# Kernel tuning notes

Measured on AMD Instinct MI355X. Metric: run time of the kernel, lower is better.

Reference implementation:

```python
import jax, jax.numpy as jnp
import numpy as np

BS, NQ, NK = 4096, 21, 7   # batch, num_neg queries, 7 keys (weekdays)
E = 512                     # key_size == query_size
H = 512                     # hidden_size
NEG_INF = -1e9


def setup_inputs() -> dict:
    key = jax.random.key(0)
    ks = jax.random.split(key, 6)
    sq = 1.0 / np.sqrt(E)
    sh = 1.0 / np.sqrt(H)
    return {
        "queries": jax.random.normal(ks[0], (BS, NQ, E), jnp.float32),
        "keys": jax.random.normal(ks[1], (BS, NK, E), jnp.float32),
        "wq_w": jax.random.normal(ks[2], (H, E), jnp.float32) * sq,
        "wq_b": jnp.zeros((H,), jnp.float32),
        "wk_w": jax.random.normal(ks[3], (H, E), jnp.float32) * sq,
        "wk_b": jnp.zeros((H,), jnp.float32),
        "wv_w": jax.random.normal(ks[4], (1, H), jnp.float32) * sh,
        "wv_b": jnp.zeros((1,), jnp.float32),
        "cum_subs_masks": jax.random.randint(ks[5], (BS, 1, NK, 1), 0, 2).astype(jnp.int32),
        "num_neg": NQ,
    }


def reference(queries, keys, wq_w, wq_b, wk_w, wk_b, wv_w, wv_b, cum_subs_masks, num_neg):
    # dropout p=0.0 -> identity (as in eval / p=0)
    q = jnp.einsum('bqe,he->bqh', queries, wq_w) + wq_b          # (bs,21,H)
    k = jnp.einsum('bke,he->bkh', keys, wk_w) + wk_b             # (bs,7,H)
    # additive score: broadcast q over keys, k over queries
    t = jnp.tanh(q[:, :, None, :] + k[:, None, :, :])            # (bs,21,7,H)
    scores = jnp.einsum('bqkh,oh->bqko', t, wv_w) + wv_b         # (bs,21,7,1)
    scores = scores + cum_subs_masks.astype(scores.dtype) * NEG_INF
    attn_weights = jax.nn.softmax(scores, axis=-2)               # softmax over 7 keys
    # weighted sum of the RAW keys (the module multiplies by expanded `keys`)
    attn_out = jnp.einsum('bqk,bke->bqe', attn_weights[..., 0], keys)  # (bs,21,E)
    return (attn_out, attn_weights)
```

## Files before the change

kernel.cpp:

```cpp
#include <hip/hip_runtime.h>
#include <hip/hip_bf16.h>

#define BS_   4096
#define NQ_   21
#define NK_   7
#define E_    512
#define MQ_   (BS_*NQ_)
#define MK_   (BS_*NK_)
#define MT1_  (MQ_/128)
#define MT2_  (MK_/128)
#define SCALE_ 2.88539008177792681f

typedef __attribute__((ext_vector_type(8))) short bf16x8;
typedef __attribute__((ext_vector_type(4))) float f32x4;
typedef __attribute__((ext_vector_type(8))) unsigned short u16x8;

__device__ __forceinline__ unsigned int cvt_pk_bf16(float lo, float hi){
  unsigned int r;
  asm("v_cvt_pk_bf16_f32 %0, %1, %2" : "=v"(r) : "v"(lo), "v"(hi));
  return r;
}
__device__ __forceinline__ float bf2f(unsigned short h){
  return __builtin_bit_cast(float, (unsigned int)h << 16);
}
__device__ __forceinline__ void gload_lds16(const void* g, void* l){
  __builtin_amdgcn_global_load_lds(
      (const __attribute__((address_space(1))) unsigned int*)g,
      (__attribute__((address_space(3))) unsigned int*)l, 16, 0, 0);
}

__global__ __launch_bounds__(256) void cast_weights(
    const float* __restrict__ wq, const float* __restrict__ wk,
    unsigned int* __restrict__ oq, unsigned int* __restrict__ ok)
{
  int i = blockIdx.x * 256 + threadIdx.x;
  float4 a = ((const float4*)wq)[i];
  float4 b = ((const float4*)wk)[i];
  uint2 ua = { cvt_pk_bf16(a.x, a.y), cvt_pk_bf16(a.z, a.w) };
  uint2 ub = { cvt_pk_bf16(b.x, b.y), cvt_pk_bf16(b.z, b.w) };
  ((uint2*)oq)[i] = ua;
  ((uint2*)ok)[i] = ub;
}

__global__ __launch_bounds__(256)
void gemm_proj(const float* __restrict__ Aq, const float* __restrict__ Ak,
               const unsigned short* __restrict__ Bq, const unsigned short* __restrict__ Bk,
               const float* __restrict__ bq, const float* __restrict__ bk,
               unsigned short* __restrict__ Cq, unsigned short* __restrict__ Ck)
{
  __shared__ char Asm[3][128 * 64];
  __shared__ char Bsm[3][128 * 64];

  const int tid  = threadIdx.x;
  const int lane = tid & 63;
  const int w    = tid >> 6;
  const int wr   = w >> 1, wc = w & 1;

  const int orig = (int)blockIdx.x;
  const int j    = orig >> 3;
  int       mt   = (j >> 2) * 8 + (orig & 7);
  const int nt   = j & 3;

  const float* A; const unsigned short* Bw; const float* bias; unsigned short* C;
  if (mt < MT1_){ A = Aq; Bw = Bq; bias = bq; C = Cq; }
  else          { A = Ak; Bw = Bk; bias = bk; C = Ck; mt -= MT1_; }

  const long m0 = (long)mt << 7;
  const int  n0 = nt << 7;
  const char* Abyte = (const char*)(A + m0 * E_);
  const char* Bbyte = (const char*)Bw;

  long asrc[4]; int adst[4];
#pragma unroll
  for (int i = 0; i < 4; ++i){
    const int c   = tid + i * 256;
    const int row = c >> 3;
    const int sl  = c & 7;
    asrc[i] = (long)row * (E_ * 4) + sl * 16;
    adst[i] = row * 64 + (((sl & 6) * 8) ^ (((row >> 1) & 3) << 4)) + (sl & 1) * 8;
  }
  long bsrc[2]; int bdst[2];
#pragma unroll
  for (int i = 0; i < 2; ++i){
    const int c   = tid + i * 256;
    const int row = c >> 2;
    const int sl  = c & 3;
    bsrc[i] = (long)(n0 + row) * (E_ * 2) + ((sl * 16) ^ (((row >> 1) & 3) << 4));
    bdst[i] = c * 16;
  }

  int aoff[4], boff[4];
#pragma unroll
  for (int m = 0; m < 4; ++m){
    const int r = wr * 64 + m * 16 + (lane & 15);
    aoff[m] = r * 64 + ((16 * (lane >> 4)) ^ (((r >> 1) & 3) << 4));
  }
#pragma unroll
  for (int n = 0; n < 4; ++n){
    const int r = wc * 64 + n * 16 + (lane & 15);
    boff[n] = r * 64 + ((16 * (lane >> 4)) ^ (((r >> 1) & 3) << 4));
  }

  f32x4 acc[4][4];
  const f32x4 z4 = {0.f, 0.f, 0.f, 0.f};
#pragma unroll
  for (int m = 0; m < 4; ++m)
#pragma unroll
    for (int n = 0; n < 4; ++n) acc[m][n] = z4;

#define STAGE_LOADS(av, T) do { \
  _Pragma("unroll") for (int i_ = 0; i_ < 4; ++i_) \
    av[i_] = *(const float4*)(Abyte + asrc[i_] + (long)(T) * 128); \
} while(0)

#define STAGE_B(BUF, T) do { \
  _Pragma("unroll") for (int i_ = 0; i_ < 2; ++i_) \
    gload_lds16(Bbyte + bsrc[i_] + (long)(T) * 64, Bsm[BUF] + bdst[i_]); \
} while(0)

#define WRITE_A(BUF, av) do { \
  _Pragma("unroll") for (int i_ = 0; i_ < 4; ++i_){ \
    uint2 u_ = { cvt_pk_bf16(av[i_].x, av[i_].y), cvt_pk_bf16(av[i_].z, av[i_].w) }; \
    *(uint2*)(Asm[BUF] + adst[i_]) = u_; \
  } \
} while(0)

#define COMPUTE(BUF) do { \
  bf16x8 af_[4], bfr_[4]; \
  _Pragma("unroll") for (int m_ = 0; m_ < 4; ++m_) af_[m_]  = *(const bf16x8*)(Asm[BUF] + aoff[m_]); \
  _Pragma("unroll") for (int n_ = 0; n_ < 4; ++n_) bfr_[n_] = *(const bf16x8*)(Bsm[BUF] + boff[n_]); \
  _Pragma("unroll") for (int m_ = 0; m_ < 4; ++m_) \
    _Pragma("unroll") for (int n_ = 0; n_ < 4; ++n_) \
      acc[m_][n_] = __builtin_amdgcn_mfma_f32_16x16x32_bf16(af_[m_], bfr_[n_], acc[m_][n_], 0, 0, 0); \
} while(0)

#define BARRIER() do { \
  asm volatile("" ::: "memory"); \
  __builtin_amdgcn_s_barrier(); \
  asm volatile("" ::: "memory"); \
} while(0)

  float4 avA[4], avB[4];

  STAGE_LOADS(avA, 0);  STAGE_B(0, 0);
  STAGE_LOADS(avB, 1);  STAGE_B(1, 1);
  asm volatile("s_waitcnt vmcnt(6)" ::: "memory");
  WRITE_A(0, avA);

#pragma unroll
  for (int t = 0; t < 14; ++t){
    const int cur = t % 3, nx1 = (t + 1) % 3, nx2 = (t + 2) % 3;
    asm volatile("s_waitcnt vmcnt(2)" ::: "memory");
    if ((t & 1) == 0) WRITE_A(nx1, avB); else WRITE_A(nx1, avA);
    asm volatile("s_waitcnt lgkmcnt(0)" ::: "memory");
    BARRIER();
    if ((t & 1) == 0) STAGE_LOADS(avA, t + 2); else STAGE_LOADS(avB, t + 2);
    STAGE_B(nx2, t + 2);
    COMPUTE(cur);
  }
  {
    asm volatile("s_waitcnt vmcnt(2)" ::: "memory");
    WRITE_A(0 , avB);
    asm volatile("s_waitcnt lgkmcnt(0)" ::: "memory");
    BARRIER();
    COMPUTE(2 );
  }
  {
    asm volatile("s_waitcnt vmcnt(0)" ::: "memory");
    BARRIER();
    COMPUTE(0 );
  }

#undef STAGE_LOADS
#undef STAGE_B
#undef WRITE_A
#undef COMPUTE
#undef BARRIER

  const int ccol0 = n0 + wc * 64 + (lane & 15);
  float bvs[4];
#pragma unroll
  for (int n = 0; n < 4; ++n) bvs[n] = bias[ccol0 + n * 16] * SCALE_;
#pragma unroll
  for (int m = 0; m < 4; ++m){
    const long rbase = m0 + wr * 64 + m * 16 + (lane >> 4) * 4;
#pragma unroll
    for (int n = 0; n < 4; ++n){
      const long col = ccol0 + n * 16;
      float v0 = fmaf(acc[m][n][0], SCALE_, bvs[n]);
      float v1 = fmaf(acc[m][n][1], SCALE_, bvs[n]);
      float v2 = fmaf(acc[m][n][2], SCALE_, bvs[n]);
      float v3 = fmaf(acc[m][n][3], SCALE_, bvs[n]);
      unsigned int u01 = cvt_pk_bf16(v0, v1);
      unsigned int u23 = cvt_pk_bf16(v2, v3);
      C[(rbase + 0) * E_ + col] = (unsigned short)(u01 & 0xffffu);
      C[(rbase + 1) * E_ + col] = (unsigned short)(u01 >> 16);
      C[(rbase + 2) * E_ + col] = (unsigned short)(u23 & 0xffffu);
      C[(rbase + 3) * E_ + col] = (unsigned short)(u23 >> 16);
    }
  }
}

__global__ __launch_bounds__(256, 2)
void attn_fused(const unsigned short* __restrict__ qp,
                const unsigned short* __restrict__ kp,
                const float* __restrict__ keys,
                const float* __restrict__ wv, const float* __restrict__ wvb,
                const int* __restrict__ mask,
                float* __restrict__ out0, float* __restrict__ out1)
{
  const int lane = threadIdx.x & 63;
  const int b    = blockIdx.x * 4 + (threadIdx.x >> 6);

  float wvr[8];
  *(float4*)&wvr[0] = ((const float4*)wv)[lane * 2];
  *(float4*)&wvr[4] = ((const float4*)wv)[lane * 2 + 1];

  float kf[NK_][8];
#pragma unroll
  for (int k = 0; k < NK_; ++k){
    u16x8 u = *(const u16x8*)(kp + ((long)b * NK_ + k) * E_ + lane * 8);
#pragma unroll
    for (int j = 0; j < 8; ++j) kf[k][j] = bf2f((unsigned short)u[j]);
  }
  float kr[NK_][8];
#pragma unroll
  for (int k = 0; k < NK_; ++k){
    const float4* p = (const float4*)(keys + ((long)b * NK_ + k) * E_ + lane * 8);
    *(float4*)&kr[k][0] = p[0];
    *(float4*)&kr[k][4] = p[1];
  }

  float wsum = ((wvr[0] + wvr[1]) + (wvr[2] + wvr[3])) + ((wvr[4] + wvr[5]) + (wvr[6] + wvr[7]));
#pragma unroll
  for (int off = 32; off; off >>= 1) wsum += __shfl_xor(wsum, off, 64);

  const float vb = wvb[0];
  float base[NK_];
#pragma unroll
  for (int k = 0; k < NK_; ++k)
    base[k] = (wsum + vb) + (float)mask[b * NK_ + k] * (-1e9f);

  const unsigned short* qrow = qp + (long)b * NQ_ * E_ + lane * 8;
  u16x8 qv = *(const u16x8*)qrow;

  float4* o0 = (float4*)(out0 + (long)b * NQ_ * E_) + lane * 2;
  float*  o1 = out1 + (long)b * (NQ_ * NK_);

  for (int qi = 0; qi < NQ_; ++qi){
    u16x8 qn = qv;
    if (qi < NQ_ - 1) qn = *(const u16x8*)(qrow + (qi + 1) * E_);

    float qf[8];
#pragma unroll
    for (int j = 0; j < 8; ++j) qf[j] = bf2f((unsigned short)qv[j]);
    qv = qn;

    float acc[NK_];
#pragma unroll
    for (int k = 0; k < NK_; ++k){
      float a = 0.f;
#pragma unroll
      for (int j = 0; j < 8; ++j){
        float x = qf[j] + kf[k][j];
        float e = __builtin_amdgcn_exp2f(x);
        float r = __builtin_amdgcn_rcpf(e + 1.0f);
        a = fmaf(wvr[j], r, a);
      }
      acc[k] = a;
    }
#pragma unroll
    for (int k = 0; k < NK_; ++k){
      float a = acc[k];
#pragma unroll
      for (int off = 32; off; off >>= 1) a += __shfl_xor(a, off, 64);
      acc[k] = a;
    }
    float sc[NK_], mx = -3.4e38f;
#pragma unroll
    for (int k = 0; k < NK_; ++k){ sc[k] = fmaf(-2.f, acc[k], base[k]); mx = fmaxf(mx, sc[k]); }
    float sum = 0.f;
#pragma unroll
    for (int k = 0; k < NK_; ++k){ sc[k] = __expf(sc[k] - mx); sum += sc[k]; }
    const float inv = __builtin_amdgcn_rcpf(sum);
    float wgt[NK_];
#pragma unroll
    for (int k = 0; k < NK_; ++k) wgt[k] = sc[k] * inv;

    float wsel = wgt[0];
#pragma unroll
    for (int k = 1; k < NK_; ++k) wsel = (lane == k) ? wgt[k] : wsel;
    if (lane < NK_) o1[qi * NK_ + lane] = wsel;

    float4 lo = {0.f,0.f,0.f,0.f}, hi = {0.f,0.f,0.f,0.f};
#pragma unroll
    for (int k = 0; k < NK_; ++k){
      lo.x = fmaf(wgt[k], kr[k][0], lo.x);
      lo.y = fmaf(wgt[k], kr[k][1], lo.y);
      lo.z = fmaf(wgt[k], kr[k][2], lo.z);
      lo.w = fmaf(wgt[k], kr[k][3], lo.w);
      hi.x = fmaf(wgt[k], kr[k][4], hi.x);
      hi.y = fmaf(wgt[k], kr[k][5], hi.y);
      hi.z = fmaf(wgt[k], kr[k][6], hi.z);
      hi.w = fmaf(wgt[k], kr[k][7], hi.w);
    }
    o0[qi * 128 + 0] = lo;
    o0[qi * 128 + 1] = hi;
  }
}

extern "C" void kernel_launch(void* const* d_in, const int* in_sizes, int n_in,
                              void* d_out, int out_size, void* d_ws, size_t ws_size,
                              hipStream_t stream)
{
  const float* queries = (const float*)d_in[0];
  const float* keys    = (const float*)d_in[1];
  const float* wq_w    = (const float*)d_in[2];
  const float* wq_b    = (const float*)d_in[3];
  const float* wk_w    = (const float*)d_in[4];
  const float* wk_b    = (const float*)d_in[5];
  const float* wv_w    = (const float*)d_in[6];
  const float* wv_b    = (const float*)d_in[7];
  const int*   mask    = (const int*)d_in[8];
  (void)in_sizes; (void)n_in; (void)out_size; (void)ws_size;

  float* out0 = (float*)d_out;
  float* out1 = out0 + (long)MQ_ * E_;

  char* ws = (char*)d_ws;
  unsigned short* wqb = (unsigned short*)ws;
  unsigned short* wkb = (unsigned short*)(ws + 512 * 512 * 2);
  unsigned short* qb  = (unsigned short*)(ws + (1 << 20));
  unsigned short* kb  = qb + (size_t)MQ_ * E_;

  cast_weights<<<dim3(256), dim3(256), 0, stream>>>(wq_w, wk_w, (unsigned int*)wqb, (unsigned int*)wkb);
  gemm_proj<<<dim3((MT1_ + MT2_) * 4), dim3(256), 0, stream>>>(
      queries, keys, wqb, wkb, wq_b, wk_b, qb, kb);
  attn_fused<<<dim3(BS_ / 4), dim3(256), 0, stream>>>(qb, kb, keys, wv_w, wv_b, mask, out0, out1);
}
```

Before: 249.0 us.

## Restructure projection GEMM to 64-row tiles with B fragments loaded directly into registers

The projection GEMM moves from 128x128 tiles with triple-buffered LDS for both operands to 64x256 tiles. Each wave owns a 64-column slice and reads its weight fragments straight from global memory into registers, one k-step ahead. Only the A tile still goes through LDS, now double-buffered and smaller, which cuts LDS traffic and footprint and may allow higher occupancy. The cost is that weight fragments are re-read from global or L2 by every block instead of being shared through LDS, and the grid shape changes.

```diff
diff --git a/kernel.cpp b/kernel.cpp
--- a/kernel.cpp
+++ b/kernel.cpp
@@ -7,8 +7,9 @@
 #define E_    512
 #define MQ_   (BS_*NQ_)
 #define MK_   (BS_*NK_)
-#define MT1_  (MQ_/128)
-#define MT2_  (MK_/128)
+#define MTQ_  (MQ_/64)
+#define MTK_  (MK_/64)
+#define MTT_  (MTQ_+MTK_)
 #define SCALE_ 2.88539008177792681f
 
 typedef __attribute__((ext_vector_type(8))) short bf16x8;
@@ -22,11 +23,6 @@
 }
 __device__ __forceinline__ float bf2f(unsigned short h){
   return __builtin_bit_cast(float, (unsigned int)h << 16);
-}
-__device__ __forceinline__ void gload_lds16(const void* g, void* l){
-  __builtin_amdgcn_global_load_lds(
-      (const __attribute__((address_space(1))) unsigned int*)g,
-      (__attribute__((address_space(3))) unsigned int*)l, 16, 0, 0);
 }
 
 __global__ __launch_bounds__(256) void cast_weights(
@@ -48,58 +44,41 @@
                const float* __restrict__ bq, const float* __restrict__ bk,
                unsigned short* __restrict__ Cq, unsigned short* __restrict__ Ck)
 {
-  __shared__ char Asm[3][128 * 64];
-  __shared__ char Bsm[3][128 * 64];
+  __shared__ char Asm[2][64 * 64];
 
   const int tid  = threadIdx.x;
   const int lane = tid & 63;
   const int w    = tid >> 6;
-  const int wr   = w >> 1, wc = w & 1;
-
-  const int orig = (int)blockIdx.x;
-  const int j    = orig >> 3;
-  int       mt   = (j >> 2) * 8 + (orig & 7);
-  const int nt   = j & 3;
+
+  const int bid = (int)blockIdx.x;
+  const int j   = bid >> 3;
+  int       mt  = (j >> 1) * 8 + (bid & 7);
+  const int ntb = j & 1;
 
   const float* A; const unsigned short* Bw; const float* bias; unsigned short* C;
-  if (mt < MT1_){ A = Aq; Bw = Bq; bias = bq; C = Cq; }
-  else          { A = Ak; Bw = Bk; bias = bk; C = Ck; mt -= MT1_; }
-
-  const long m0 = (long)mt << 7;
-  const int  n0 = nt << 7;
+  if (mt < MTQ_){ A = Aq; Bw = Bq; bias = bq; C = Cq; }
+  else          { A = Ak; Bw = Bk; bias = bk; C = Ck; mt -= MTQ_; }
+
+  const long m0  = (long)mt << 6;
+  const int  n0w = ntb * 256 + w * 64;
   const char* Abyte = (const char*)(A + m0 * E_);
-  const char* Bbyte = (const char*)Bw;
-
-  long asrc[4]; int adst[4];
-#pragma unroll
-  for (int i = 0; i < 4; ++i){
+
+  long asrc[2]; int adst[2];
+#pragma unroll
+  for (int i = 0; i < 2; ++i){
     const int c   = tid + i * 256;
     const int row = c >> 3;
     const int sl  = c & 7;
     asrc[i] = (long)row * (E_ * 4) + sl * 16;
     adst[i] = row * 64 + (((sl & 6) * 8) ^ (((row >> 1) & 3) << 4)) + (sl & 1) * 8;
   }
-  long bsrc[2]; int bdst[2];
-#pragma unroll
-  for (int i = 0; i < 2; ++i){
-    const int c   = tid + i * 256;
-    const int row = c >> 2;
-    const int sl  = c & 3;
-    bsrc[i] = (long)(n0 + row) * (E_ * 2) + ((sl * 16) ^ (((row >> 1) & 3) << 4));
-    bdst[i] = c * 16;
-  }
-
-  int aoff[4], boff[4];
+  int aoff[4];
 #pragma unroll
   for (int m = 0; m < 4; ++m){
-    const int r = wr * 64 + m * 16 + (lane & 15);
+    const int r = m * 16 + (lane & 15);
     aoff[m] = r * 64 + ((16 * (lane >> 4)) ^ (((r >> 1) & 3) << 4));
   }
-#pragma unroll
-  for (int n = 0; n < 4; ++n){
-    const int r = wc * 64 + n * 16 + (lane & 15);
-    boff[n] = r * 64 + ((16 * (lane >> 4)) ^ (((r >> 1) & 3) << 4));
-  }
+  const unsigned short* Bp = Bw + (long)(n0w + (lane & 15)) * E_ + (lane >> 4) * 8;
 
   f32x4 acc[4][4];
   const f32x4 z4 = {0.f, 0.f, 0.f, 0.f};
@@ -108,82 +87,86 @@
 #pragma unroll
     for (int n = 0; n < 4; ++n) acc[m][n] = z4;
 
-#define STAGE_LOADS(av, T) do { \
-  _Pragma("unroll") for (int i_ = 0; i_ < 4; ++i_) \
+  bf16x8 bfrC[4], bfrN[4];
+  float4 avA[2], avB[2];
+
+#define LOAD_A(av, T) do { \
+  _Pragma("unroll") for (int i_ = 0; i_ < 2; ++i_) \
     av[i_] = *(const float4*)(Abyte + asrc[i_] + (long)(T) * 128); \
 } while(0)
 
-#define STAGE_B(BUF, T) do { \
-  _Pragma("unroll") for (int i_ = 0; i_ < 2; ++i_) \
-    gload_lds16(Bbyte + bsrc[i_] + (long)(T) * 64, Bsm[BUF] + bdst[i_]); \
+#define LOAD_B(dst, T) do { \
+  _Pragma("unroll") for (int n_ = 0; n_ < 4; ++n_) \
+    dst[n_] = *(const bf16x8*)(Bp + (long)n_ * 16 * E_ + (T) * 32); \
 } while(0)
 
 #define WRITE_A(BUF, av) do { \
-  _Pragma("unroll") for (int i_ = 0; i_ < 4; ++i_){ \
+  _Pragma("unroll") for (int i_ = 0; i_ < 2; ++i_){ \
     uint2 u_ = { cvt_pk_bf16(av[i_].x, av[i_].y), cvt_pk_bf16(av[i_].z, av[i_].w) }; \
     *(uint2*)(Asm[BUF] + adst[i_]) = u_; \
   } \
 } while(0)
 
 #define COMPUTE(BUF) do { \
-  bf16x8 af_[4], bfr_[4]; \
-  _Pragma("unroll") for (int m_ = 0; m_ < 4; ++m_) af_[m_]  = *(const bf16x8*)(Asm[BUF] + aoff[m_]); \
-  _Pragma("unroll") for (int n_ = 0; n_ < 4; ++n_) bfr_[n_] = *(const bf16x8*)(Bsm[BUF] + boff[n_]); \
+  bf16x8 af_[4]; \
+  _Pragma("unroll") for (int m_ = 0; m_ < 4; ++m_) \
+    af_[m_] = *(const bf16x8*)(Asm[BUF] + aoff[m_]); \
   _Pragma("unroll") for (int m_ = 0; m_ < 4; ++m_) \
     _Pragma("unroll") for (int n_ = 0; n_ < 4; ++n_) \
-      acc[m_][n_] = __builtin_amdgcn_mfma_f32_16x16x32_bf16(af_[m_], bfr_[n_], acc[m_][n_], 0, 0, 0); \
-} while(0)
-
-#define BARRIER() do { \
-  asm volatile("" ::: "memory"); \
+      acc[m_][n_] = __builtin_amdgcn_mfma_f32_16x16x32_bf16(af_[m_], bfrC[n_], acc[m_][n_], 0, 0, 0); \
+} while(0)
+
+#define BAR() do { \
+  asm volatile("s_waitcnt lgkmcnt(0)" ::: "memory"); \
   __builtin_amdgcn_s_barrier(); \
-  asm volatile("" ::: "memory"); \
-} while(0)
-
-  float4 avA[4], avB[4];
-
-  STAGE_LOADS(avA, 0);  STAGE_B(0, 0);
-  STAGE_LOADS(avB, 1);  STAGE_B(1, 1);
-  asm volatile("s_waitcnt vmcnt(6)" ::: "memory");
+  __builtin_amdgcn_sched_barrier(0); \
+} while(0)
+
+#define STEP(T, AVISS, AVWR) do { \
+  LOAD_A(AVISS, (T) + 2); \
+  LOAD_B(bfrN, (T) + 1); \
+  COMPUTE((T) & 1); \
+  WRITE_A(((T) + 1) & 1, AVWR); \
+  BAR(); \
+  _Pragma("unroll") for (int n_ = 0; n_ < 4; ++n_) bfrC[n_] = bfrN[n_]; \
+} while(0)
+
+  LOAD_A(avA, 0);
+  LOAD_A(avB, 1);
+  LOAD_B(bfrC, 0);
   WRITE_A(0, avA);
-
-#pragma unroll
-  for (int t = 0; t < 14; ++t){
-    const int cur = t % 3, nx1 = (t + 1) % 3, nx2 = (t + 2) % 3;
-    asm volatile("s_waitcnt vmcnt(2)" ::: "memory");
-    if ((t & 1) == 0) WRITE_A(nx1, avB); else WRITE_A(nx1, avA);
-    asm volatile("s_waitcnt lgkmcnt(0)" ::: "memory");
-    BARRIER();
-    if ((t & 1) == 0) STAGE_LOADS(avA, t + 2); else STAGE_LOADS(avB, t + 2);
-    STAGE_B(nx2, t + 2);
-    COMPUTE(cur);
+  BAR();
+
+#pragma unroll
+  for (int tp = 0; tp < 7; ++tp){
+    const int t = tp * 2;
+    STEP(t,     avA, avB);
+    STEP(t + 1, avB, avA);
   }
   {
-    asm volatile("s_waitcnt vmcnt(2)" ::: "memory");
-    WRITE_A(0 , avB);
-    asm volatile("s_waitcnt lgkmcnt(0)" ::: "memory");
-    BARRIER();
-    COMPUTE(2 );
-  }
-  {
-    asm volatile("s_waitcnt vmcnt(0)" ::: "memory");
-    BARRIER();
-    COMPUTE(0 );
-  }
-
-#undef STAGE_LOADS
-#undef STAGE_B
+    LOAD_B(bfrN, 15);
+    COMPUTE(0);
+    WRITE_A(1, avB);
+    BAR();
+#pragma unroll
+    for (int n_ = 0; n_ < 4; ++n_) bfrC[n_] = bfrN[n_];
+  }
+  COMPUTE(1);
+
+#undef LOAD_A
+#undef LOAD_B
 #undef WRITE_A
 #undef COMPUTE
-#undef BARRIER
-
-  const int ccol0 = n0 + wc * 64 + (lane & 15);
+#undef BAR
+#undef STEP
+
+  const int ccol0 = n0w + (lane & 15);
   float bvs[4];
 #pragma unroll
   for (int n = 0; n < 4; ++n) bvs[n] = bias[ccol0 + n * 16] * SCALE_;
 #pragma unroll
   for (int m = 0; m < 4; ++m){
-    const long rbase = m0 + wr * 64 + m * 16 + (lane >> 4) * 4;
+    const long rbase = m0 + m * 16 + (lane >> 4) * 4;
 #pragma unroll
     for (int n = 0; n < 4; ++n){
       const long col = ccol0 + n * 16;
@@ -334,7 +317,7 @@
   unsigned short* kb  = qb + (size_t)MQ_ * E_;
 
   cast_weights<<<dim3(256), dim3(256), 0, stream>>>(wq_w, wk_w, (unsigned int*)wqb, (unsigned int*)wkb);
-  gemm_proj<<<dim3((MT1_ + MT2_) * 4), dim3(256), 0, stream>>>(
+  gemm_proj<<<dim3(MTT_ * 2), dim3(256), 0, stream>>>(
       queries, keys, wqb, wkb, wq_b, wk_b, qb, kb);
   attn_fused<<<dim3(BS_ / 4), dim3(256), 0, stream>>>(qb, kb, keys, wv_w, wv_b, mask, out0, out1);
 }
```

After: 293.4 us. +17.8%, slower.

## Factor tanh exp into per-query and per-key exponentials and split queries across waves

Applied to the files above, without the earlier changes.

The attention kernel rewrites exp2(q+k) as exp2(q)*exp2(k). The key exponentials are computed once per batch row and the query exponentials once per query, which removes the 7x repeated exp per element and leaves an FMA plus a reciprocal in the inner loop. Each batch row is now handled by two waves that split the 21 queries 11/10, doubling the grid to add parallelism. The cost is that each wave reloads and re-exponentiates the keys. Separate exponentials can also overflow to inf for large projected values, though rcp of inf still gives the correct tanh limit.

```diff
diff --git a/kernel.cpp b/kernel.cpp
--- a/kernel.cpp
+++ b/kernel.cpp
@@ -150,25 +150,26 @@
 #pragma unroll
   for (int t = 0; t < 14; ++t){
     const int cur = t % 3, nx1 = (t + 1) % 3, nx2 = (t + 2) % 3;
+    (void)cur;
     asm volatile("s_waitcnt vmcnt(2)" ::: "memory");
     if ((t & 1) == 0) WRITE_A(nx1, avB); else WRITE_A(nx1, avA);
     asm volatile("s_waitcnt lgkmcnt(0)" ::: "memory");
     BARRIER();
     if ((t & 1) == 0) STAGE_LOADS(avA, t + 2); else STAGE_LOADS(avB, t + 2);
     STAGE_B(nx2, t + 2);
-    COMPUTE(cur);
+    COMPUTE(t % 3);
   }
   {
     asm volatile("s_waitcnt vmcnt(2)" ::: "memory");
-    WRITE_A(0 , avB);
+    WRITE_A(0, avB);
     asm volatile("s_waitcnt lgkmcnt(0)" ::: "memory");
     BARRIER();
-    COMPUTE(2 );
+    COMPUTE(2);
   }
   {
     asm volatile("s_waitcnt vmcnt(0)" ::: "memory");
     BARRIER();
-    COMPUTE(0 );
+    COMPUTE(0);
   }
 
 #undef STAGE_LOADS
@@ -210,23 +211,27 @@
                 float* __restrict__ out0, float* __restrict__ out1)
 {
   const int lane = threadIdx.x & 63;
-  const int b    = blockIdx.x * 4 + (threadIdx.x >> 6);
+  const int w    = threadIdx.x >> 6;
+  const long b   = (long)blockIdx.x * 2 + (w >> 1);
+  const int  q0  = (w & 1) * 11;
+  const int  q1  = (w & 1) ? NQ_ : 11;
 
   float wvr[8];
   *(float4*)&wvr[0] = ((const float4*)wv)[lane * 2];
   *(float4*)&wvr[4] = ((const float4*)wv)[lane * 2 + 1];
 
-  float kf[NK_][8];
+  float ek[NK_][8];
 #pragma unroll
   for (int k = 0; k < NK_; ++k){
-    u16x8 u = *(const u16x8*)(kp + ((long)b * NK_ + k) * E_ + lane * 8);
-#pragma unroll
-    for (int j = 0; j < 8; ++j) kf[k][j] = bf2f((unsigned short)u[j]);
+    u16x8 u = *(const u16x8*)(kp + (b * NK_ + k) * E_ + lane * 8);
+#pragma unroll
+    for (int j = 0; j < 8; ++j)
+      ek[k][j] = __builtin_amdgcn_exp2f(bf2f((unsigned short)u[j]));
   }
   float kr[NK_][8];
 #pragma unroll
   for (int k = 0; k < NK_; ++k){
-    const float4* p = (const float4*)(keys + ((long)b * NK_ + k) * E_ + lane * 8);
+    const float4* p = (const float4*)(keys + (b * NK_ + k) * E_ + lane * 8);
     *(float4*)&kr[k][0] = p[0];
     *(float4*)&kr[k][4] = p[1];
   }
@@ -241,19 +246,20 @@
   for (int k = 0; k < NK_; ++k)
     base[k] = (wsum + vb) + (float)mask[b * NK_ + k] * (-1e9f);
 
-  const unsigned short* qrow = qp + (long)b * NQ_ * E_ + lane * 8;
-  u16x8 qv = *(const u16x8*)qrow;
-
-  float4* o0 = (float4*)(out0 + (long)b * NQ_ * E_) + lane * 2;
-  float*  o1 = out1 + (long)b * (NQ_ * NK_);
-
-  for (int qi = 0; qi < NQ_; ++qi){
+  const unsigned short* qrow = qp + b * NQ_ * E_ + lane * 8;
+  u16x8 qv = *(const u16x8*)(qrow + q0 * E_);
+
+  float4* o0 = (float4*)(out0 + b * NQ_ * E_) + lane * 2;
+  float*  o1 = out1 + b * (NQ_ * NK_);
+
+  for (int qi = q0; qi < q1; ++qi){
     u16x8 qn = qv;
-    if (qi < NQ_ - 1) qn = *(const u16x8*)(qrow + (qi + 1) * E_);
-
-    float qf[8];
-#pragma unroll
-    for (int j = 0; j < 8; ++j) qf[j] = bf2f((unsigned short)qv[j]);
+    if (qi < q1 - 1) qn = *(const u16x8*)(qrow + (qi + 1) * E_);
+
+    float eq[8];
+#pragma unroll
+    for (int j = 0; j < 8; ++j)
+      eq[j] = __builtin_amdgcn_exp2f(bf2f((unsigned short)qv[j]));
     qv = qn;
 
     float acc[NK_];
@@ -262,9 +268,8 @@
       float a = 0.f;
 #pragma unroll
       for (int j = 0; j < 8; ++j){
-        float x = qf[j] + kf[k][j];
-        float e = __builtin_amdgcn_exp2f(x);
-        float r = __builtin_amdgcn_rcpf(e + 1.0f);
+        float t = fmaf(eq[j], ek[k][j], 1.0f);
+        float r = __builtin_amdgcn_rcpf(t);
         a = fmaf(wvr[j], r, a);
       }
       acc[k] = a;
@@ -336,5 +341,5 @@
   cast_weights<<<dim3(256), dim3(256), 0, stream>>>(wq_w, wk_w, (unsigned int*)wqb, (unsigned int*)wkb);
   gemm_proj<<<dim3((MT1_ + MT2_) * 4), dim3(256), 0, stream>>>(
       queries, keys, wqb, wkb, wq_b, wk_b, qb, kb);
-  attn_fused<<<dim3(BS_ / 4), dim3(256), 0, stream>>>(qb, kb, keys, wv_w, wv_b, mask, out0, out1);
-}
+  attn_fused<<<dim3(BS_ / 2), dim3(256), 0, stream>>>(qb, kb, keys, wv_w, wv_b, mask, out0, out1);
+}
```

Measured after the change: 268.1 us. 1.08x slower.
